# Optimization experiments

Hardware: AMD Instinct MI355X
Metric: run time of the kernel (lower is better)

Reference implementation:

```python
import jax, jax.numpy as jnp
import numpy as np

H = 128  # hidden_size


def lstm_layer(x, Wih, Whh, bih, bhh):
    """Unidirectional LSTM layer, batch_first input x: [B, T, I] -> [B, T, H].
    PyTorch gate order: i, f, g, o."""
    B = x.shape[0]
    # precompute input projections as one big GEMM: [B, T, 4H]
    xp = jnp.einsum('bti,gi->btg', x, Wih) + bih + bhh
    xp = jnp.transpose(xp, (1, 0, 2))  # [T, B, 4H]
    h0 = jnp.zeros((B, H), x.dtype)
    c0 = jnp.zeros((B, H), x.dtype)

    def step(carry, xp_t):
        h, c = carry
        gates = xp_t + h @ Whh.T  # [B, 4H]
        i, f, g, o = jnp.split(gates, 4, axis=-1)
        i = jax.nn.sigmoid(i)
        f = jax.nn.sigmoid(f)
        g = jnp.tanh(g)
        o = jax.nn.sigmoid(o)
        c = f * c + i * g
        h = o * jnp.tanh(c)
        return (h, c), h

    (_, _), ys = jax.lax.scan(step, (h0, c0), xp)
    return jnp.transpose(ys, (1, 0, 2))  # [B, T, H]


def setup_inputs() -> dict:
    key = jax.random.key(0)
    ks = jax.random.split(key, 13)
    s = 0.05
    inp = {
        'x': jax.random.normal(ks[0], (8, 1, 102400), jnp.float32),
        'Wih0': jax.random.normal(ks[1], (4 * H, 1), jnp.float32) * s,
        'Whh0': jax.random.normal(ks[2], (4 * H, H), jnp.float32) * s,
        'bih0': jnp.zeros((4 * H,), jnp.float32),
        'bhh0': jnp.zeros((4 * H,), jnp.float32).at[H:2 * H].set(1.0),
        'Wih1': jax.random.normal(ks[3], (4 * H, H), jnp.float32) * s,
        'Whh1': jax.random.normal(ks[4], (4 * H, H), jnp.float32) * s,
        'bih1': jnp.zeros((4 * H,), jnp.float32),
        'bhh1': jnp.zeros((4 * H,), jnp.float32).at[H:2 * H].set(1.0),
        'fcW1': jax.random.normal(ks[5], (H // 2, H), jnp.float32) * s,
        'fcb1': jnp.zeros((H // 2,), jnp.float32),
        'fcW2': jax.random.normal(ks[6], (11, H // 2), jnp.float32) * s,
        'fcb2': jnp.zeros((11,), jnp.float32),
    }
    return inp


def reference(x, Wih0, Whh0, bih0, bhh0, Wih1, Whh1, bih1, bhh1,
              fcW1, fcb1, fcW2, fcb2):
    # x: [B, 1, L] -> [B, L, 1]  (transpose(1, 2))
    x = jnp.transpose(x, (0, 2, 1))
    h1 = lstm_layer(x, Wih0, Whh0, bih0, bhh0)   # [B, T, H]
    h2 = lstm_layer(h1, Wih1, Whh1, bih1, bhh1)  # [B, T, H]
    pooled = jnp.mean(h2, axis=1)                # [B, H]; dropout is identity in eval
    hid = jax.nn.relu(pooled @ fcW1.T + fcb1)    # [B, H//2]
    logits = hid @ fcW2.T + fcb2                 # [B, 11]
    return logits
```

## Files before the change

kernel.cpp:

```cpp
#include <hip/hip_runtime.h>

#define HH 128
#define G4 512
#define TT 102400
#define BB 8

typedef _Float16 v2h __attribute__((ext_vector_type(2)));

#if __has_builtin(__builtin_amdgcn_fdot2)
#define FDOT2(a, b, c) __builtin_amdgcn_fdot2((a), (b), (c), false)
#else
static __device__ __forceinline__ float fdot2_fb(v2h a, v2h b, float c) {
    return fmaf((float)a[0], (float)b[0], fmaf((float)a[1], (float)b[1], c));
}
#define FDOT2(a, b, c) fdot2_fb((a), (b), (c))
#endif

template<int CTRL>
__device__ __forceinline__ float dpp_mov(float v) {
    return __int_as_float(
        __builtin_amdgcn_update_dpp(0, __float_as_int(v), CTRL, 0xF, 0xF, true));
}

__device__ __forceinline__ float tanh_f(float x) {
    return fmaf(2.0f, __builtin_amdgcn_rcpf(1.0f + __expf(-2.0f * x)), -1.0f);
}

static __device__ __forceinline__ void bar_lds() {
    __builtin_amdgcn_sched_barrier(0);
    asm volatile("s_waitcnt lgkmcnt(0)" ::: "memory");
    __builtin_amdgcn_s_barrier();
    __builtin_amdgcn_sched_barrier(0);
}

union HI { int i; v2h h; };

__device__ __forceinline__ float dotred(const v2h w[8][8],
                                        const _Float16* __restrict__ hsl,
                                        bool bp1, bool bp2, bool bp3) {
    const int4* hp4 = (const int4*)hsl;
    int4 ha = hp4[0], hb = hp4[1];
    int hp[8] = {ha.x, ha.y, ha.z, ha.w, hb.x, hb.y, hb.z, hb.w};
    float acc[8];
#pragma unroll
    for (int r = 0; r < 8; ++r) acc[r] = 0.f;
#pragma unroll
    for (int i = 0; i < 8; ++i) {
        HI u; u.i = hp[i];
#pragma unroll
        for (int r = 0; r < 8; ++r) acc[r] = FDOT2(w[r][i], u.h, acc[r]);
    }
    float b0[4];
#pragma unroll
    for (int m = 0; m < 4; ++m) {
        float send = bp1 ? acc[2 * m] : acc[2 * m + 1];
        float keep = bp1 ? acc[2 * m + 1] : acc[2 * m];
        b0[m] = keep + dpp_mov<0xB1>(send);
    }
    float d0[2];
#pragma unroll
    for (int i = 0; i < 2; ++i) {
        float send = bp2 ? b0[i] : b0[i + 2];
        float keep = bp2 ? b0[i + 2] : b0[i];
        d0[i] = keep + dpp_mov<0x4E>(send);
    }
    float send = bp3 ? d0[0] : d0[1];
    float keep = bp3 ? d0[1] : d0[0];
    return keep + dpp_mov<0x141>(send);
}

__device__ __forceinline__ void load_w8h(const float* __restrict__ W,
                                         int Q, int j, v2h w[8][8]) {
#pragma unroll
    for (int r = 0; r < 8; ++r) {
        int row = 2 * Q + (r & 1) + 128 * (r >> 1);
        const float4* rp = (const float4*)(W + (size_t)row * HH + 16 * j);
#pragma unroll
        for (int i = 0; i < 4; ++i) {
            float4 f = rp[i];
            w[r][2 * i]     = (v2h){(_Float16)f.x, (_Float16)f.y};
            w[r][2 * i + 1] = (v2h){(_Float16)f.z, (_Float16)f.w};
        }
    }
}

__global__ void __launch_bounds__(512, 2)
lstm_slot_kernel(
    const float* __restrict__ x,
    const float* __restrict__ Wih0, const float* __restrict__ Whh0,
    const float* __restrict__ bih0, const float* __restrict__ bhh0,
    const float* __restrict__ Wih1, const float* __restrict__ Whh1,
    const float* __restrict__ bih1, const float* __restrict__ bhh1,
    float* __restrict__ h1s, float* __restrict__ c1s,
    float* __restrict__ h2s, float* __restrict__ c2s,
    double* __restrict__ pooled,
    _Float16* __restrict__ h1ring,
    float* __restrict__ xpring,
    int c, int chunkT, int nchunks)
{
    __shared__ __align__(32) _Float16 hh[2 * HH];
    const int t = threadIdx.x;
    const int Q = t >> 3;
    const int j = t & 7;
    const bool bp1 = ((j ^ (j >> 2)) & 1) != 0;
    const bool bp2 = ((j ^ (j >> 1)) & 1) != 0;
    const bool bp3 = ((j >> 2) & 1) != 0;
    const int cellj = bp1 ? 1 : 0;
    const int gatej = (bp2 ? 2 : 0) + (bp3 ? 1 : 0);
    const int myc   = 2 * Q + cellj;
    const int myrow = myc + 128 * gatej;
    const bool owner = (gatej == 0);
    const bool isg = (gatej == 2);
    const float fe = isg ? -2.f : -1.f;
    const float fm = isg ?  2.f :  1.f;
    const float fa = isg ? -1.f :  0.f;

    if (blockIdx.x < 16) {
        const bool isA = (blockIdx.x < 8);
        const int cc = isA ? c : (c - 2);
        if (cc < 0 || cc >= nchunks) return;
        const int b = blockIdx.x & 7;

        v2h w[8][8];
        load_w8h(isA ? Whh0 : Whh1, Q, j, w);
        float bias_l = 0.f, wih_l = 0.f;
        if (isA) { bias_l = bih0[myrow] + bhh0[myrow]; wih_l = Wih0[myrow]; }

        float* hst = isA ? h1s : h2s;
        float* cst = isA ? c1s : c2s;
        float c_reg = cst[b * HH + myc];
        if (t < HH) hh[t] = (_Float16)hst[b * HH + t];

        _Float16* ringp = h1ring + ((size_t)((c & 1) * BB + b)) * (size_t)chunkT * HH;
        const float4* xb4 = (const float4*)(x + (size_t)b * TT + (size_t)cc * chunkT);
        const float* xps = xpring
            + ((size_t)((cc & 1) * BB + b)) * (size_t)chunkT * G4 + 4 * myc + gatej;

        const int nt4 = chunkT >> 2;
        float4 xq = {0, 0, 0, 0};
        float xpc[4] = {0, 0, 0, 0};
        if (isA) xq = xb4[0];
        else {
#pragma unroll
            for (int u = 0; u < 4; ++u) xpc[u] = xps[(size_t)u * G4];
        }
        double pacc = 0.0;
        float hfin = 0.f;
        bar_lds();

        for (int t4 = 0; t4 < nt4; ++t4) {
            float4 xqn = {0, 0, 0, 0};
            float xpn[4] = {0, 0, 0, 0};
            if (isA) {
                if (t4 + 1 < nt4) xqn = xb4[t4 + 1];
            } else if (t4 + 1 < nt4) {
#pragma unroll
                for (int u = 0; u < 4; ++u)
                    xpn[u] = xps[(size_t)(t4 * 4 + 4 + u) * G4];
            }
#pragma unroll
            for (int u = 0; u < 4; ++u) {
                const int buf = u & 1;
                float sfin = dotred(w, hh + buf * HH + 16 * j, bp1, bp2, bp3);
                float pre;
                if (isA) {
                    float xt = (u == 0) ? xq.x : (u == 1) ? xq.y
                             : (u == 2) ? xq.z : xq.w;
                    pre = fmaf(xt, wih_l, sfin + bias_l);
                } else {
                    pre = sfin + xpc[u];
                }
                float e  = __expf(pre * fe);
                float rr = __builtin_amdgcn_rcpf(1.0f + e);
                float act = fmaf(fm, rr, fa);
                float t1 = dpp_mov<0x141>(act);
                float t2 = dpp_mov<0x4E>(act);
                float t3 = dpp_mov<0x4E>(t1);
                c_reg = fmaf(t1, c_reg, act * t2);
                float th = tanh_f(c_reg);
                float hv = t3 * th;
                hfin = hv;
                if (owner) {
                    hh[(buf ^ 1) * HH + myc] = (_Float16)hv;
                    if (isA) ringp[(size_t)(t4 * 4 + u) * HH + myc] = (_Float16)hv;
                    else     pacc += (double)hv;
                }
                bar_lds();
            }
            xq = xqn;
            if (!isA) {
#pragma unroll
                for (int u = 0; u < 4; ++u) xpc[u] = xpn[u];
            }
        }
        if (owner) {
            cst[b * HH + myc] = c_reg;
            hst[b * HH + myc] = hfin;
            if (!isA) pooled[b * HH + myc] += pacc;
        }

    } else {
        const int bc = c - 1;
        if (bc < 0 || bc >= nchunks) return;
        const int ib = blockIdx.x - 16;
        const int bb = ib >> 3;
        const int sl = ib & 7;
        v2h w[8][8];
        load_w8h(Wih1, Q, j, w);
        const float bias_l = bih1[myrow] + bhh1[myrow];
        const _Float16* hrp = h1ring
            + ((size_t)((bc & 1) * BB + bb)) * (size_t)chunkT * HH;
        float* xpw = xpring + ((size_t)((bc & 1) * BB + bb)) * (size_t)chunkT * G4;
        if (t < HH) hh[t] = hrp[(size_t)sl * HH + t];
        bar_lds();
        int pb = 0;
        for (int tt = sl; tt < chunkT; tt += 8) {
            int ttn = tt + 8;
            bool pf = (t < HH) && (ttn < chunkT);
            _Float16 hn = (_Float16)0.f;
            if (pf) hn = hrp[(size_t)ttn * HH + t];
            float sfin = dotred(w, hh + pb * HH + 16 * j, bp1, bp2, bp3);
            if (pf) hh[(pb ^ 1) * HH + t] = hn;
            xpw[(size_t)tt * G4 + 4 * myc + gatej] = sfin + bias_l;
            bar_lds();
            pb ^= 1;
        }
    }
}

__global__ void head_kernel(const double* __restrict__ pooled,
                            const float* __restrict__ fcW1, const float* __restrict__ fcb1,
                            const float* __restrict__ fcW2, const float* __restrict__ fcb2,
                            float* __restrict__ out)
{
    __shared__ float p_s[HH];
    __shared__ float hid_s[64];
    const int b = blockIdx.x, t = threadIdx.x;
    if (t < HH) p_s[t] = (float)(pooled[b * HH + t] * (1.0 / (double)TT));
    __syncthreads();
    if (t < 64) {
        float acc = fcb1[t];
#pragma unroll 8
        for (int k = 0; k < HH; ++k) acc = fmaf(p_s[k], fcW1[t * HH + k], acc);
        hid_s[t] = fmaxf(acc, 0.f);
    }
    __syncthreads();
    if (t < 11) {
        float acc = fcb2[t];
#pragma unroll
        for (int k = 0; k < 64; ++k) acc = fmaf(hid_s[k], fcW2[t * 64 + k], acc);
        out[b * 11 + t] = acc;
    }
}

extern "C" void kernel_launch(void* const* d_in, const int* in_sizes, int n_in,
                              void* d_out, int out_size, void* d_ws, size_t ws_size,
                              hipStream_t stream)
{
    const float* x    = (const float*)d_in[0];
    const float* Wih0 = (const float*)d_in[1];
    const float* Whh0 = (const float*)d_in[2];
    const float* bih0 = (const float*)d_in[3];
    const float* bhh0 = (const float*)d_in[4];
    const float* Wih1 = (const float*)d_in[5];
    const float* Whh1 = (const float*)d_in[6];
    const float* bih1 = (const float*)d_in[7];
    const float* bhh1 = (const float*)d_in[8];
    const float* fcW1 = (const float*)d_in[9];
    const float* fcb1 = (const float*)d_in[10];
    const float* fcW2 = (const float*)d_in[11];
    const float* fcb2 = (const float*)d_in[12];
    float* out = (float*)d_out;

    char* wsp = (char*)d_ws;
    float*  h1s    = (float*) (wsp + 0);
    float*  c1s    = (float*) (wsp + 4096);
    float*  h2s    = (float*) (wsp + 8192);
    float*  c2s    = (float*) (wsp + 12288);
    double* pooled = (double*)(wsp + 16384);
    const size_t STATE_BYTES = 24576;

    static const int cands[] = {800, 400, 160, 80, 40, 8};
    int chunkT = 8;
    for (int i = 0; i < 6; ++i) {
        size_t need = STATE_BYTES + (size_t)36864 * (size_t)cands[i];
        if (need <= ws_size) { chunkT = cands[i]; break; }
    }
    const int nchunks = TT / chunkT;

    _Float16* h1ring = (_Float16*)(wsp + STATE_BYTES);
    float* xpring = (float*)(wsp + STATE_BYTES + (size_t)2 * BB * chunkT * HH * 2);

    hipMemsetAsync(d_ws, 0, STATE_BYTES, stream);

    const int nslots = nchunks + 2;
    for (int c = 0; c < nslots; ++c) {
        lstm_slot_kernel<<<80, 512, 0, stream>>>(
            x, Wih0, Whh0, bih0, bhh0, Wih1, Whh1, bih1, bhh1,
            h1s, c1s, h2s, c2s, pooled, h1ring, xpring,
            c, chunkT, nchunks);
    }
    head_kernel<<<BB, 128, 0, stream>>>(pooled, fcW1, fcb1, fcW2, fcb2, out);
}
```

Before: 57.92 ms.

## Compute recurrent LSTM matvec with MFMA 16x16x32 instead of fdot2 lane reductions

The recurrent blocks now compute h·Whh with MFMA 16x16x32 f16 instructions. Each wave holds fp16 weight fragments for 16 cells across all four gates. One active lane per cell extracts its four gate sums and runs the full cell update, which replaces the fdot2-plus-DPP cross-lane reduction and the DPP gate exchange. The custom LDS barrier is replaced by __syncthreads and the xprojection prefetch is reorganised per step pair. This trades the reduction latency for MFMA latency on a serial chain, with only a quarter of lanes doing activations.

```diff
diff --git a/kernel.cpp b/kernel.cpp
--- a/kernel.cpp
+++ b/kernel.cpp
@@ -6,6 +6,10 @@
 #define BB 8
 
 typedef _Float16 v2h __attribute__((ext_vector_type(2)));
+typedef _Float16 v8h __attribute__((ext_vector_type(8)));
+typedef float    f4v __attribute__((ext_vector_type(4)));
+
+#define MFMA16(A, B, C) __builtin_amdgcn_mfma_f32_16x16x32_f16((A), (B), (C), 0, 0, 0)
 
 #if __has_builtin(__builtin_amdgcn_fdot2)
 #define FDOT2(a, b, c) __builtin_amdgcn_fdot2((a), (b), (c), false)
@@ -25,12 +29,8 @@
 __device__ __forceinline__ float tanh_f(float x) {
     return fmaf(2.0f, __builtin_amdgcn_rcpf(1.0f + __expf(-2.0f * x)), -1.0f);
 }
-
-static __device__ __forceinline__ void bar_lds() {
-    __builtin_amdgcn_sched_barrier(0);
-    asm volatile("s_waitcnt lgkmcnt(0)" ::: "memory");
-    __builtin_amdgcn_s_barrier();
-    __builtin_amdgcn_sched_barrier(0);
+__device__ __forceinline__ float sigm_f(float x) {
+    return __builtin_amdgcn_rcpf(1.0f + __expf(-x));
 }
 
 union HI { int i; v2h h; };
@@ -100,20 +100,6 @@
 {
     __shared__ __align__(32) _Float16 hh[2 * HH];
     const int t = threadIdx.x;
-    const int Q = t >> 3;
-    const int j = t & 7;
-    const bool bp1 = ((j ^ (j >> 2)) & 1) != 0;
-    const bool bp2 = ((j ^ (j >> 1)) & 1) != 0;
-    const bool bp3 = ((j >> 2) & 1) != 0;
-    const int cellj = bp1 ? 1 : 0;
-    const int gatej = (bp2 ? 2 : 0) + (bp3 ? 1 : 0);
-    const int myc   = 2 * Q + cellj;
-    const int myrow = myc + 128 * gatej;
-    const bool owner = (gatej == 0);
-    const bool isg = (gatej == 2);
-    const float fe = isg ? -2.f : -1.f;
-    const float fm = isg ?  2.f :  1.f;
-    const float fa = isg ? -1.f :  0.f;
 
     if (blockIdx.x < 16) {
         const bool isA = (blockIdx.x < 8);
@@ -121,87 +107,155 @@
         if (cc < 0 || cc >= nchunks) return;
         const int b = blockIdx.x & 7;
 
-        v2h w[8][8];
-        load_w8h(isA ? Whh0 : Whh1, Q, j, w);
-        float bias_l = 0.f, wih_l = 0.f;
-        if (isA) { bias_l = bih0[myrow] + bhh0[myrow]; wih_l = Wih0[myrow]; }
+        const int l   = t & 63;
+        const int wv  = t >> 6;
+        const int lhi = l >> 4;
+        const int lq  = l & 3;
+        const int koff = 8 * lhi;
+        const bool act_lane = ((l & 12) == 0);
+        const int cellw = 16 * wv + 4 * lhi + lq;
+        const bool s0_ = (l & 1) != 0, s1_ = (l & 2) != 0;
+
+        const float* Wc = isA ? Whh0 : Whh1;
+        v8h af[4][4];
+#pragma unroll
+        for (int g = 0; g < 4; ++g) {
+            const float* wr = Wc + (size_t)(16 * wv + 128 * g + (l & 15)) * HH;
+#pragma unroll
+            for (int kt = 0; kt < 4; ++kt) {
+                const f4v* p = (const f4v*)(wr + 32 * kt + koff);
+                f4v fa = p[0], fb = p[1];
+                v8h v;
+                v[0] = (_Float16)fa[0]; v[1] = (_Float16)fa[1];
+                v[2] = (_Float16)fa[2]; v[3] = (_Float16)fa[3];
+                v[4] = (_Float16)fb[0]; v[5] = (_Float16)fb[1];
+                v[6] = (_Float16)fb[2]; v[7] = (_Float16)fb[3];
+                af[g][kt] = v;
+            }
+        }
+        f4v cin[4] = {{0,0,0,0},{0,0,0,0},{0,0,0,0},{0,0,0,0}};
+        float wih_[4] = {0.f, 0.f, 0.f, 0.f};
+        if (isA) {
+#pragma unroll
+            for (int g = 0; g < 4; ++g) {
+#pragma unroll
+                for (int r = 0; r < 4; ++r) {
+                    int row = 16 * wv + 128 * g + 4 * lhi + r;
+                    cin[g][r] = bih0[row] + bhh0[row];
+                }
+                wih_[g] = Wih0[cellw + 128 * g];
+            }
+        }
 
         float* hst = isA ? h1s : h2s;
         float* cst = isA ? c1s : c2s;
-        float c_reg = cst[b * HH + myc];
+        float c_reg = cst[b * HH + cellw];
         if (t < HH) hh[t] = (_Float16)hst[b * HH + t];
 
-        _Float16* ringp = h1ring + ((size_t)((c & 1) * BB + b)) * (size_t)chunkT * HH;
-        const float4* xb4 = (const float4*)(x + (size_t)b * TT + (size_t)cc * chunkT);
-        const float* xps = xpring
-            + ((size_t)((cc & 1) * BB + b)) * (size_t)chunkT * G4 + 4 * myc + gatej;
-
-        const int nt4 = chunkT >> 2;
-        float4 xq = {0, 0, 0, 0};
-        float xpc[4] = {0, 0, 0, 0};
-        if (isA) xq = xb4[0];
-        else {
-#pragma unroll
-            for (int u = 0; u < 4; ++u) xpc[u] = xps[(size_t)u * G4];
-        }
+        _Float16* rp = h1ring + ((size_t)((c & 1) * BB + b)) * (size_t)chunkT * HH;
+        const float* xrow = x + (size_t)b * TT + (size_t)cc * chunkT;
+        const float* xpp = xpring
+            + ((size_t)((cc & 1) * BB + b)) * (size_t)chunkT * G4 + 4 * cellw;
+
+        float xt0 = 0.f, xt1 = 0.f;
+        f4v xp0 = {0,0,0,0}, xp1 = {0,0,0,0};
+        if (isA) { xt0 = xrow[0]; xt1 = xrow[1]; }
+        else if (act_lane) {
+            xp0 = *(const f4v*)(xpp);
+            xp1 = *(const f4v*)(xpp + G4);
+        }
+        const float* xrp = xrow + 2;
+        const float* xpn = xpp + 2 * (size_t)G4;
+
         double pacc = 0.0;
         float hfin = 0.f;
-        bar_lds();
-
-        for (int t4 = 0; t4 < nt4; ++t4) {
-            float4 xqn = {0, 0, 0, 0};
-            float xpn[4] = {0, 0, 0, 0};
+        __syncthreads();
+
+#define CHAIN_STEP(PAR, XT, XP) do {                                          \
+        const _Float16* hb_ = hh + (PAR) * HH + koff;                         \
+        v8h b0_ = *(const v8h*)(hb_);                                         \
+        v8h b1_ = *(const v8h*)(hb_ + 32);                                    \
+        v8h b2_ = *(const v8h*)(hb_ + 64);                                    \
+        v8h b3_ = *(const v8h*)(hb_ + 96);                                    \
+        f4v a0_ = MFMA16(af[0][0], b0_, cin[0]);                              \
+        f4v a1_ = MFMA16(af[1][0], b0_, cin[1]);                              \
+        f4v a2_ = MFMA16(af[2][0], b0_, cin[2]);                              \
+        f4v a3_ = MFMA16(af[3][0], b0_, cin[3]);                              \
+        a0_ = MFMA16(af[0][1], b1_, a0_); a1_ = MFMA16(af[1][1], b1_, a1_);   \
+        a2_ = MFMA16(af[2][1], b1_, a2_); a3_ = MFMA16(af[3][1], b1_, a3_);   \
+        a0_ = MFMA16(af[0][2], b2_, a0_); a1_ = MFMA16(af[1][2], b2_, a1_);   \
+        a2_ = MFMA16(af[2][2], b2_, a2_); a3_ = MFMA16(af[3][2], b2_, a3_);   \
+        a0_ = MFMA16(af[0][3], b3_, a0_); a1_ = MFMA16(af[1][3], b3_, a1_);   \
+        a2_ = MFMA16(af[2][3], b3_, a2_); a3_ = MFMA16(af[3][3], b3_, a3_);   \
+        float q01_, q23_, si_, sf_, sg2_, so_;                                \
+        q01_ = s0_ ? a0_[1] : a0_[0]; q23_ = s0_ ? a0_[3] : a0_[2];           \
+        si_  = s1_ ? q23_ : q01_;                                             \
+        q01_ = s0_ ? a1_[1] : a1_[0]; q23_ = s0_ ? a1_[3] : a1_[2];           \
+        sf_  = s1_ ? q23_ : q01_;                                             \
+        q01_ = s0_ ? a2_[1] : a2_[0]; q23_ = s0_ ? a2_[3] : a2_[2];           \
+        sg2_ = s1_ ? q23_ : q01_;                                             \
+        q01_ = s0_ ? a3_[1] : a3_[0]; q23_ = s0_ ? a3_[3] : a3_[2];           \
+        so_  = s1_ ? q23_ : q01_;                                             \
+        if (act_lane) {                                                       \
+            float pi_, pf_, pg_, po_;                                         \
+            if (isA) {                                                        \
+                pi_ = fmaf(XT, wih_[0], si_);                                 \
+                pf_ = fmaf(XT, wih_[1], sf_);                                 \
+                pg_ = fmaf(XT, wih_[2], sg2_);                                \
+                po_ = fmaf(XT, wih_[3], so_);                                 \
+            } else {                                                          \
+                pi_ = si_ + XP[0]; pf_ = sf_ + XP[1];                         \
+                pg_ = sg2_ + XP[2]; po_ = so_ + XP[3];                        \
+            }                                                                 \
+            float gi_ = sigm_f(pi_), gf_ = sigm_f(pf_);                       \
+            float gg_ = tanh_f(pg_), go_ = sigm_f(po_);                       \
+            c_reg = fmaf(gf_, c_reg, gi_ * gg_);                              \
+            float hv_ = go_ * tanh_f(c_reg);                                  \
+            hfin = hv_;                                                       \
+            hh[(((PAR) ^ 1)) * HH + cellw] = (_Float16)hv_;                   \
+            if (isA) rp[cellw] = (_Float16)hv_;                               \
+            else     pacc += (double)hv_;                                     \
+        }                                                                     \
+        rp += HH;                                                             \
+        __syncthreads();                                                      \
+    } while (0)
+
+        for (int s = 0; s < chunkT; s += 2) {
+            float xt2 = 0.f, xt3 = 0.f;
+            f4v xp2 = {0,0,0,0}, xp3 = {0,0,0,0};
+            const bool p2 = (s + 2 < chunkT);
             if (isA) {
-                if (t4 + 1 < nt4) xqn = xb4[t4 + 1];
-            } else if (t4 + 1 < nt4) {
-#pragma unroll
-                for (int u = 0; u < 4; ++u)
-                    xpn[u] = xps[(size_t)(t4 * 4 + 4 + u) * G4];
+                if (p2) { xt2 = xrp[0]; xt3 = xrp[1]; }
+            } else if (act_lane && p2) {
+                xp2 = *(const f4v*)(xpn);
+                xp3 = *(const f4v*)(xpn + G4);
             }
-#pragma unroll
-            for (int u = 0; u < 4; ++u) {
-                const int buf = u & 1;
-                float sfin = dotred(w, hh + buf * HH + 16 * j, bp1, bp2, bp3);
-                float pre;
-                if (isA) {
-                    float xt = (u == 0) ? xq.x : (u == 1) ? xq.y
-                             : (u == 2) ? xq.z : xq.w;
-                    pre = fmaf(xt, wih_l, sfin + bias_l);
-                } else {
-                    pre = sfin + xpc[u];
-                }
-                float e  = __expf(pre * fe);
-                float rr = __builtin_amdgcn_rcpf(1.0f + e);
-                float act = fmaf(fm, rr, fa);
-                float t1 = dpp_mov<0x141>(act);
-                float t2 = dpp_mov<0x4E>(act);
-                float t3 = dpp_mov<0x4E>(t1);
-                c_reg = fmaf(t1, c_reg, act * t2);
-                float th = tanh_f(c_reg);
-                float hv = t3 * th;
-                hfin = hv;
-                if (owner) {
-                    hh[(buf ^ 1) * HH + myc] = (_Float16)hv;
-                    if (isA) ringp[(size_t)(t4 * 4 + u) * HH + myc] = (_Float16)hv;
-                    else     pacc += (double)hv;
-                }
-                bar_lds();
-            }
-            xq = xqn;
-            if (!isA) {
-#pragma unroll
-                for (int u = 0; u < 4; ++u) xpc[u] = xpn[u];
-            }
-        }
-        if (owner) {
-            cst[b * HH + myc] = c_reg;
-            hst[b * HH + myc] = hfin;
-            if (!isA) pooled[b * HH + myc] += pacc;
+            CHAIN_STEP(0, xt0, xp0);
+            CHAIN_STEP(1, xt1, xp1);
+            xt0 = xt2; xt1 = xt3; xp0 = xp2; xp1 = xp3;
+            xrp += 2; xpn += 2 * (size_t)G4;
+        }
+#undef CHAIN_STEP
+
+        if (act_lane) {
+            cst[b * HH + cellw] = c_reg;
+            hst[b * HH + cellw] = hfin;
+            if (!isA) pooled[b * HH + cellw] += pacc;
         }
 
     } else {
         const int bc = c - 1;
         if (bc < 0 || bc >= nchunks) return;
+        const int Q = t >> 3;
+        const int j = t & 7;
+        const bool bp1 = ((j ^ (j >> 2)) & 1) != 0;
+        const bool bp2 = ((j ^ (j >> 1)) & 1) != 0;
+        const bool bp3 = ((j >> 2) & 1) != 0;
+        const int cellj = bp1 ? 1 : 0;
+        const int gatej = (bp2 ? 2 : 0) + (bp3 ? 1 : 0);
+        const int myc   = 2 * Q + cellj;
+        const int myrow = myc + 128 * gatej;
+
         const int ib = blockIdx.x - 16;
         const int bb = ib >> 3;
         const int sl = ib & 7;
@@ -212,7 +266,7 @@
             + ((size_t)((bc & 1) * BB + bb)) * (size_t)chunkT * HH;
         float* xpw = xpring + ((size_t)((bc & 1) * BB + bb)) * (size_t)chunkT * G4;
         if (t < HH) hh[t] = hrp[(size_t)sl * HH + t];
-        bar_lds();
+        __syncthreads();
         int pb = 0;
         for (int tt = sl; tt < chunkT; tt += 8) {
             int ttn = tt + 8;
@@ -222,7 +276,7 @@
             float sfin = dotred(w, hh + pb * HH + 16 * j, bp1, bp2, bp3);
             if (pf) hh[(pb ^ 1) * HH + t] = hn;
             xpw[(size_t)tt * G4 + 4 * myc + gatej] = sfin + bias_l;
-            bar_lds();
+            __syncthreads();
             pb ^= 1;
         }
     }
```

New measurement: 59.50 ms. 2.7% more time.

## Batch all sequences per recurrent block and compute recurrence with MFMA

Applied to the files above, without the earlier changes.

The recurrent layer blocks now handle all 8 batch rows in a single 256-thread workgroup, using 16x16x32 f16 MFMA instructions with Whh held in registers as A-fragments, in place of one 512-thread block per batch row using fdot2 and DPP reductions. Each lane evaluates the gate nonlinearities for 4 cells directly, and x is staged into LDS for the chunk. The layer-1 input-projection blocks are split into two halves over cells, giving 130 blocks of 256 threads. This trades per-step cross-lane reduction work and many blocks for a denser matrix-core step with one barrier. The risk is a longer per-step serial MFMA dependency chain on a single CU per layer.

```diff
diff --git a/kernel.cpp b/kernel.cpp
--- a/kernel.cpp
+++ b/kernel.cpp
@@ -4,8 +4,14 @@
 #define G4 512
 #define TT 102400
 #define BB 8
+#define XS 801
+#define HS2 144
 
 typedef _Float16 v2h __attribute__((ext_vector_type(2)));
+typedef _Float16 v8h __attribute__((ext_vector_type(8)));
+typedef float    f4v __attribute__((ext_vector_type(4)));
+
+#define MFMA16(A, B, C) __builtin_amdgcn_mfma_f32_16x16x32_f16((A), (B), (C), 0, 0, 0)
 
 #if __has_builtin(__builtin_amdgcn_fdot2)
 #define FDOT2(a, b, c) __builtin_amdgcn_fdot2((a), (b), (c), false)
@@ -25,12 +31,8 @@
 __device__ __forceinline__ float tanh_f(float x) {
     return fmaf(2.0f, __builtin_amdgcn_rcpf(1.0f + __expf(-2.0f * x)), -1.0f);
 }
-
-static __device__ __forceinline__ void bar_lds() {
-    __builtin_amdgcn_sched_barrier(0);
-    asm volatile("s_waitcnt lgkmcnt(0)" ::: "memory");
-    __builtin_amdgcn_s_barrier();
-    __builtin_amdgcn_sched_barrier(0);
+__device__ __forceinline__ float sigm_f(float x) {
+    return __builtin_amdgcn_rcpf(1.0f + __expf(-x));
 }
 
 union HI { int i; v2h h; };
@@ -70,10 +72,10 @@
 }
 
 __device__ __forceinline__ void load_w8h(const float* __restrict__ W,
-                                         int Q, int j, v2h w[8][8]) {
+                                         int Q, int j, int ch, v2h w[8][8]) {
 #pragma unroll
     for (int r = 0; r < 8; ++r) {
-        int row = 2 * Q + (r & 1) + 128 * (r >> 1);
+        int row = 64 * ch + 2 * Q + (r & 1) + 128 * (r >> 1);
         const float4* rp = (const float4*)(W + (size_t)row * HH + 16 * j);
 #pragma unroll
         for (int i = 0; i < 4; ++i) {
@@ -84,7 +86,7 @@
     }
 }
 
-__global__ void __launch_bounds__(512, 2)
+__global__ void __launch_bounds__(256, 1)
 lstm_slot_kernel(
     const float* __restrict__ x,
     const float* __restrict__ Wih0, const float* __restrict__ Whh0,
@@ -98,131 +100,258 @@
     float* __restrict__ xpring,
     int c, int chunkT, int nchunks)
 {
-    __shared__ __align__(32) _Float16 hh[2 * HH];
+    __shared__ __align__(16) _Float16 hh2[2][BB * HS2];
+    __shared__ __align__(16) float x_lds[BB * XS];
     const int t = threadIdx.x;
-    const int Q = t >> 3;
-    const int j = t & 7;
-    const bool bp1 = ((j ^ (j >> 2)) & 1) != 0;
-    const bool bp2 = ((j ^ (j >> 1)) & 1) != 0;
-    const bool bp3 = ((j >> 2) & 1) != 0;
-    const int cellj = bp1 ? 1 : 0;
-    const int gatej = (bp2 ? 2 : 0) + (bp3 ? 1 : 0);
-    const int myc   = 2 * Q + cellj;
-    const int myrow = myc + 128 * gatej;
-    const bool owner = (gatej == 0);
-    const bool isg = (gatej == 2);
-    const float fe = isg ? -2.f : -1.f;
-    const float fm = isg ?  2.f :  1.f;
-    const float fa = isg ? -1.f :  0.f;
-
-    if (blockIdx.x < 16) {
-        const bool isA = (blockIdx.x < 8);
+
+    if (blockIdx.x < 2) {
+        const bool isA = (blockIdx.x == 0);
         const int cc = isA ? c : (c - 2);
         if (cc < 0 || cc >= nchunks) return;
-        const int b = blockIdx.x & 7;
-
-        v2h w[8][8];
-        load_w8h(isA ? Whh0 : Whh1, Q, j, w);
-        float bias_l = 0.f, wih_l = 0.f;
-        if (isA) { bias_l = bih0[myrow] + bhh0[myrow]; wih_l = Wih0[myrow]; }
+
+        const int l   = t & 63;
+        const int w   = t >> 6;
+        const int lr  = l & 15;
+        const int lhi = l >> 4;
+        const int bb  = lr & 7;
+        const int hs  = lr >> 3;
+        const int ccb = 32 * w + 16 * hs + 4 * lhi;
+
+        const float* Wc = isA ? Whh0 : Whh1;
+        v8h af[4][2][4];
+#pragma unroll
+        for (int g = 0; g < 4; ++g)
+#pragma unroll
+            for (int h2 = 0; h2 < 2; ++h2)
+#pragma unroll
+                for (int kt = 0; kt < 4; ++kt) {
+                    const float* wr = Wc + (size_t)(32 * w + 16 * h2 + lr + 128 * g) * HH
+                                    + 32 * kt + 8 * lhi;
+                    f4v fa = *(const f4v*)wr, fb = *(const f4v*)(wr + 4);
+                    v8h v;
+                    v[0] = (_Float16)fa[0]; v[1] = (_Float16)fa[1];
+                    v[2] = (_Float16)fa[2]; v[3] = (_Float16)fa[3];
+                    v[4] = (_Float16)fb[0]; v[5] = (_Float16)fb[1];
+                    v[6] = (_Float16)fb[2]; v[7] = (_Float16)fb[3];
+                    af[g][h2][kt] = v;
+                }
+
+        f4v cin[4][2];
+#pragma unroll
+        for (int g = 0; g < 4; ++g)
+#pragma unroll
+            for (int h2 = 0; h2 < 2; ++h2) cin[g][h2] = (f4v){0.f, 0.f, 0.f, 0.f};
+        float wih[4][4];
+#pragma unroll
+        for (int r = 0; r < 4; ++r)
+#pragma unroll
+            for (int g = 0; g < 4; ++g) wih[r][g] = 0.f;
+        if (isA) {
+#pragma unroll
+            for (int g = 0; g < 4; ++g)
+#pragma unroll
+                for (int h2 = 0; h2 < 2; ++h2)
+#pragma unroll
+                    for (int r = 0; r < 4; ++r) {
+                        int row = 32 * w + 16 * h2 + 4 * lhi + r + 128 * g;
+                        cin[g][h2][r] = bih0[row] + bhh0[row];
+                    }
+#pragma unroll
+            for (int r = 0; r < 4; ++r)
+#pragma unroll
+                for (int g = 0; g < 4; ++g) wih[r][g] = Wih0[ccb + r + 128 * g];
+        }
 
         float* hst = isA ? h1s : h2s;
         float* cst = isA ? c1s : c2s;
-        float c_reg = cst[b * HH + myc];
-        if (t < HH) hh[t] = (_Float16)hst[b * HH + t];
-
-        _Float16* ringp = h1ring + ((size_t)((c & 1) * BB + b)) * (size_t)chunkT * HH;
-        const float4* xb4 = (const float4*)(x + (size_t)b * TT + (size_t)cc * chunkT);
+        float cr0 = cst[bb * HH + ccb + 0];
+        float cr1 = cst[bb * HH + ccb + 1];
+        float cr2 = cst[bb * HH + ccb + 2];
+        float cr3 = cst[bb * HH + ccb + 3];
+        float hl0 = 0.f, hl1 = 0.f, hl2 = 0.f, hl3 = 0.f;
+        float pac0 = 0.f, pac1 = 0.f, pac2 = 0.f, pac3 = 0.f;
+
+        for (int i = t; i < BB * HH; i += 256)
+            hh2[0][(i >> 7) * HS2 + (i & 127)] = (_Float16)hst[i];
+        if (isA) {
+            for (int b_ = 0; b_ < 8; ++b_)
+                for (int tp = t; tp < chunkT; tp += 256)
+                    x_lds[b_ * XS + tp] = x[(size_t)b_ * TT + (size_t)cc * chunkT + tp];
+        }
+
+        _Float16* rp = h1ring + ((size_t)((c & 1) * BB + bb)) * (size_t)chunkT * HH + ccb;
         const float* xps = xpring
-            + ((size_t)((cc & 1) * BB + b)) * (size_t)chunkT * G4 + 4 * myc + gatej;
-
-        const int nt4 = chunkT >> 2;
-        float4 xq = {0, 0, 0, 0};
-        float xpc[4] = {0, 0, 0, 0};
-        if (isA) xq = xb4[0];
-        else {
-#pragma unroll
-            for (int u = 0; u < 4; ++u) xpc[u] = xps[(size_t)u * G4];
-        }
-        double pacc = 0.0;
-        float hfin = 0.f;
-        bar_lds();
-
-        for (int t4 = 0; t4 < nt4; ++t4) {
-            float4 xqn = {0, 0, 0, 0};
-            float xpn[4] = {0, 0, 0, 0};
-            if (isA) {
-                if (t4 + 1 < nt4) xqn = xb4[t4 + 1];
-            } else if (t4 + 1 < nt4) {
-#pragma unroll
-                for (int u = 0; u < 4; ++u)
-                    xpn[u] = xps[(size_t)(t4 * 4 + 4 + u) * G4];
-            }
-#pragma unroll
-            for (int u = 0; u < 4; ++u) {
-                const int buf = u & 1;
-                float sfin = dotred(w, hh + buf * HH + 16 * j, bp1, bp2, bp3);
-                float pre;
-                if (isA) {
-                    float xt = (u == 0) ? xq.x : (u == 1) ? xq.y
-                             : (u == 2) ? xq.z : xq.w;
-                    pre = fmaf(xt, wih_l, sfin + bias_l);
-                } else {
-                    pre = sfin + xpc[u];
-                }
-                float e  = __expf(pre * fe);
-                float rr = __builtin_amdgcn_rcpf(1.0f + e);
-                float act = fmaf(fm, rr, fa);
-                float t1 = dpp_mov<0x141>(act);
-                float t2 = dpp_mov<0x4E>(act);
-                float t3 = dpp_mov<0x4E>(t1);
-                c_reg = fmaf(t1, c_reg, act * t2);
-                float th = tanh_f(c_reg);
-                float hv = t3 * th;
-                hfin = hv;
-                if (owner) {
-                    hh[(buf ^ 1) * HH + myc] = (_Float16)hv;
-                    if (isA) ringp[(size_t)(t4 * 4 + u) * HH + myc] = (_Float16)hv;
-                    else     pacc += (double)hv;
-                }
-                bar_lds();
-            }
-            xq = xqn;
-            if (!isA) {
-#pragma unroll
-                for (int u = 0; u < 4; ++u) xpc[u] = xpn[u];
-            }
-        }
-        if (owner) {
-            cst[b * HH + myc] = c_reg;
-            hst[b * HH + myc] = hfin;
-            if (!isA) pooled[b * HH + myc] += pacc;
+            + ((size_t)((cc & 1) * BB + bb)) * (size_t)chunkT * G4 + 4 * ccb;
+
+        f4v xc0 = {0,0,0,0}, xc1 = {0,0,0,0}, xc2 = {0,0,0,0}, xc3 = {0,0,0,0};
+        f4v xn0 = {0,0,0,0}, xn1 = {0,0,0,0}, xn2 = {0,0,0,0}, xn3 = {0,0,0,0};
+        if (!isA) {
+            xc0 = *(const f4v*)(xps);     xc1 = *(const f4v*)(xps + 4);
+            xc2 = *(const f4v*)(xps + 8); xc3 = *(const f4v*)(xps + 12);
+        }
+        __syncthreads();
+
+#define CSTEP(PB, S, SN, XC0,XC1,XC2,XC3, XN0,XN1,XN2,XN3) do {               \
+        if (!isA && (SN) < chunkT) {                                          \
+            const float* q_ = xps + (size_t)(SN) * G4;                        \
+            XN0 = *(const f4v*)q_;        XN1 = *(const f4v*)(q_ + 4);        \
+            XN2 = *(const f4v*)(q_ + 8);  XN3 = *(const f4v*)(q_ + 12);       \
+        }                                                                     \
+        const _Float16* hb_ = &hh2[PB][bb * HS2 + 8 * lhi];                   \
+        v8h B0_ = *(const v8h*)(hb_);                                         \
+        v8h B1_ = *(const v8h*)(hb_ + 32);                                    \
+        v8h B2_ = *(const v8h*)(hb_ + 64);                                    \
+        v8h B3_ = *(const v8h*)(hb_ + 96);                                    \
+        f4v a00_ = cin[0][0], a01_ = cin[0][1], a10_ = cin[1][0],             \
+            a11_ = cin[1][1], a20_ = cin[2][0], a21_ = cin[2][1],             \
+            a30_ = cin[3][0], a31_ = cin[3][1];                               \
+        a00_ = MFMA16(af[0][0][0], B0_, a00_);                                \
+        a00_ = MFMA16(af[0][0][1], B1_, a00_);                                \
+        a00_ = MFMA16(af[0][0][2], B2_, a00_);                                \
+        a00_ = MFMA16(af[0][0][3], B3_, a00_);                                \
+        a10_ = MFMA16(af[1][0][0], B0_, a10_);                                \
+        a10_ = MFMA16(af[1][0][1], B1_, a10_);                                \
+        a10_ = MFMA16(af[1][0][2], B2_, a10_);                                \
+        a10_ = MFMA16(af[1][0][3], B3_, a10_);                                \
+        a20_ = MFMA16(af[2][0][0], B0_, a20_);                                \
+        a20_ = MFMA16(af[2][0][1], B1_, a20_);                                \
+        a20_ = MFMA16(af[2][0][2], B2_, a20_);                                \
+        a20_ = MFMA16(af[2][0][3], B3_, a20_);                                \
+        a30_ = MFMA16(af[3][0][0], B0_, a30_);                                \
+        a30_ = MFMA16(af[3][0][1], B1_, a30_);                                \
+        a30_ = MFMA16(af[3][0][2], B2_, a30_);                                \
+        a30_ = MFMA16(af[3][0][3], B3_, a30_);                                \
+        a01_ = MFMA16(af[0][1][0], B0_, a01_);                                \
+        a01_ = MFMA16(af[0][1][1], B1_, a01_);                                \
+        a01_ = MFMA16(af[0][1][2], B2_, a01_);                                \
+        a01_ = MFMA16(af[0][1][3], B3_, a01_);                                \
+        a11_ = MFMA16(af[1][1][0], B0_, a11_);                                \
+        a11_ = MFMA16(af[1][1][1], B1_, a11_);                                \
+        a11_ = MFMA16(af[1][1][2], B2_, a11_);                                \
+        a11_ = MFMA16(af[1][1][3], B3_, a11_);                                \
+        a21_ = MFMA16(af[2][1][0], B0_, a21_);                                \
+        a21_ = MFMA16(af[2][1][1], B1_, a21_);                                \
+        a21_ = MFMA16(af[2][1][2], B2_, a21_);                                \
+        a21_ = MFMA16(af[2][1][3], B3_, a21_);                                \
+        a31_ = MFMA16(af[3][1][0], B0_, a31_);                                \
+        a31_ = MFMA16(af[3][1][1], B1_, a31_);                                \
+        a31_ = MFMA16(af[3][1][2], B2_, a31_);                                \
+        a31_ = MFMA16(af[3][1][3], B3_, a31_);                                \
+        f4v vi_ = hs ? a01_ : a00_;  f4v vf_ = hs ? a11_ : a10_;              \
+        f4v vg_ = hs ? a21_ : a20_;  f4v vo_ = hs ? a31_ : a30_;              \
+        float xt_ = x_lds[bb * XS + (S)];                                     \
+        float h0_, h1_, h2v_, h3_;                                            \
+        {                                                                     \
+            float pi_, pf_, pg_, po_;                                         \
+            if (isA) { pi_ = fmaf(xt_, wih[0][0], vi_[0]);                    \
+                       pf_ = fmaf(xt_, wih[0][1], vf_[0]);                    \
+                       pg_ = fmaf(xt_, wih[0][2], vg_[0]);                    \
+                       po_ = fmaf(xt_, wih[0][3], vo_[0]); }                  \
+            else { pi_ = vi_[0] + XC0[0]; pf_ = vf_[0] + XC0[1];              \
+                   pg_ = vg_[0] + XC0[2]; po_ = vo_[0] + XC0[3]; }            \
+            float gi_ = sigm_f(pi_), gf_ = sigm_f(pf_);                       \
+            float gg_ = tanh_f(pg_), go_ = sigm_f(po_);                       \
+            cr0 = fmaf(gf_, cr0, gi_ * gg_);  h0_ = go_ * tanh_f(cr0);        \
+        }                                                                     \
+        {                                                                     \
+            float pi_, pf_, pg_, po_;                                         \
+            if (isA) { pi_ = fmaf(xt_, wih[1][0], vi_[1]);                    \
+                       pf_ = fmaf(xt_, wih[1][1], vf_[1]);                    \
+                       pg_ = fmaf(xt_, wih[1][2], vg_[1]);                    \
+                       po_ = fmaf(xt_, wih[1][3], vo_[1]); }                  \
+            else { pi_ = vi_[1] + XC1[0]; pf_ = vf_[1] + XC1[1];              \
+                   pg_ = vg_[1] + XC1[2]; po_ = vo_[1] + XC1[3]; }            \
+            float gi_ = sigm_f(pi_), gf_ = sigm_f(pf_);                       \
+            float gg_ = tanh_f(pg_), go_ = sigm_f(po_);                       \
+            cr1 = fmaf(gf_, cr1, gi_ * gg_);  h1_ = go_ * tanh_f(cr1);        \
+        }                                                                     \
+        {                                                                     \
+            float pi_, pf_, pg_, po_;                                         \
+            if (isA) { pi_ = fmaf(xt_, wih[2][0], vi_[2]);                    \
+                       pf_ = fmaf(xt_, wih[2][1], vf_[2]);                    \
+                       pg_ = fmaf(xt_, wih[2][2], vg_[2]);                    \
+                       po_ = fmaf(xt_, wih[2][3], vo_[2]); }                  \
+            else { pi_ = vi_[2] + XC2[0]; pf_ = vf_[2] + XC2[1];              \
+                   pg_ = vg_[2] + XC2[2]; po_ = vo_[2] + XC2[3]; }            \
+            float gi_ = sigm_f(pi_), gf_ = sigm_f(pf_);                       \
+            float gg_ = tanh_f(pg_), go_ = sigm_f(po_);                       \
+            cr2 = fmaf(gf_, cr2, gi_ * gg_);  h2v_ = go_ * tanh_f(cr2);       \
+        }                                                                     \
+        {                                                                     \
+            float pi_, pf_, pg_, po_;                                         \
+            if (isA) { pi_ = fmaf(xt_, wih[3][0], vi_[3]);                    \
+                       pf_ = fmaf(xt_, wih[3][1], vf_[3]);                    \
+                       pg_ = fmaf(xt_, wih[3][2], vg_[3]);                    \
+                       po_ = fmaf(xt_, wih[3][3], vo_[3]); }                  \
+            else { pi_ = vi_[3] + XC3[0]; pf_ = vf_[3] + XC3[1];              \
+                   pg_ = vg_[3] + XC3[2]; po_ = vo_[3] + XC3[3]; }            \
+            float gi_ = sigm_f(pi_), gf_ = sigm_f(pf_);                       \
+            float gg_ = tanh_f(pg_), go_ = sigm_f(po_);                       \
+            cr3 = fmaf(gf_, cr3, gi_ * gg_);  h3_ = go_ * tanh_f(cr3);        \
+        }                                                                     \
+        union { v2h hp[2]; unsigned long long u; } pk_;                       \
+        pk_.hp[0] = (v2h){(_Float16)h0_, (_Float16)h1_};                      \
+        pk_.hp[1] = (v2h){(_Float16)h2v_, (_Float16)h3_};                     \
+        *(unsigned long long*)(&hh2[(PB) ^ 1][bb * HS2 + ccb]) = pk_.u;       \
+        if (isA) *(unsigned long long*)(rp + (size_t)(S) * HH) = pk_.u;       \
+        else { pac0 += h0_; pac1 += h1_; pac2 += h2v_; pac3 += h3_; }         \
+        hl0 = h0_; hl1 = h1_; hl2 = h2v_; hl3 = h3_;                          \
+        __syncthreads();                                                      \
+    } while (0)
+
+        for (int s = 0; s < chunkT; s += 2) {
+            CSTEP(0, s,     s + 1, xc0, xc1, xc2, xc3, xn0, xn1, xn2, xn3);
+            CSTEP(1, s + 1, s + 2, xn0, xn1, xn2, xn3, xc0, xc1, xc2, xc3);
+        }
+#undef CSTEP
+
+        cst[bb * HH + ccb + 0] = cr0; cst[bb * HH + ccb + 1] = cr1;
+        cst[bb * HH + ccb + 2] = cr2; cst[bb * HH + ccb + 3] = cr3;
+        hst[bb * HH + ccb + 0] = hl0; hst[bb * HH + ccb + 1] = hl1;
+        hst[bb * HH + ccb + 2] = hl2; hst[bb * HH + ccb + 3] = hl3;
+        if (!isA) {
+            pooled[bb * HH + ccb + 0] += (double)pac0;
+            pooled[bb * HH + ccb + 1] += (double)pac1;
+            pooled[bb * HH + ccb + 2] += (double)pac2;
+            pooled[bb * HH + ccb + 3] += (double)pac3;
         }
 
     } else {
         const int bc = c - 1;
         if (bc < 0 || bc >= nchunks) return;
-        const int ib = blockIdx.x - 16;
-        const int bb = ib >> 3;
-        const int sl = ib & 7;
-        v2h w[8][8];
-        load_w8h(Wih1, Q, j, w);
+        const int ib = blockIdx.x - 2;
+        const int bb2 = ib >> 4;
+        const int sl = (ib >> 1) & 7;
+        const int ch = ib & 1;
+        const int Q = t >> 3;
+        const int j = t & 7;
+        const bool bp1 = ((j ^ (j >> 2)) & 1) != 0;
+        const bool bp2 = ((j ^ (j >> 1)) & 1) != 0;
+        const bool bp3 = ((j >> 2) & 1) != 0;
+        const int cellj = bp1 ? 1 : 0;
+        const int gatej = (bp2 ? 2 : 0) + (bp3 ? 1 : 0);
+        const int myc   = 64 * ch + 2 * Q + cellj;
+        const int myrow = myc + 128 * gatej;
+
+        v2h wB[8][8];
+        load_w8h(Wih1, Q, j, ch, wB);
         const float bias_l = bih1[myrow] + bhh1[myrow];
         const _Float16* hrp = h1ring
-            + ((size_t)((bc & 1) * BB + bb)) * (size_t)chunkT * HH;
-        float* xpw = xpring + ((size_t)((bc & 1) * BB + bb)) * (size_t)chunkT * G4;
-        if (t < HH) hh[t] = hrp[(size_t)sl * HH + t];
-        bar_lds();
+            + ((size_t)((bc & 1) * BB + bb2)) * (size_t)chunkT * HH;
+        float* xpw = xpring + ((size_t)((bc & 1) * BB + bb2)) * (size_t)chunkT * G4;
+        _Float16* hhB = &hh2[0][0];
+        if (t < HH) hhB[t] = hrp[(size_t)sl * HH + t];
+        __syncthreads();
         int pb = 0;
         for (int tt = sl; tt < chunkT; tt += 8) {
             int ttn = tt + 8;
             bool pf = (t < HH) && (ttn < chunkT);
             _Float16 hn = (_Float16)0.f;
             if (pf) hn = hrp[(size_t)ttn * HH + t];
-            float sfin = dotred(w, hh + pb * HH + 16 * j, bp1, bp2, bp3);
-            if (pf) hh[(pb ^ 1) * HH + t] = hn;
+            float sfin = dotred(wB, hhB + pb * HH + 16 * j, bp1, bp2, bp3);
+            if (pf) hhB[(pb ^ 1) * HH + t] = hn;
             xpw[(size_t)tt * G4 + 4 * myc + gatej] = sfin + bias_l;
-            bar_lds();
+            __syncthreads();
             pb ^= 1;
         }
     }
@@ -295,7 +424,7 @@
 
     const int nslots = nchunks + 2;
     for (int c = 0; c < nslots; ++c) {
-        lstm_slot_kernel<<<80, 512, 0, stream>>>(
+        lstm_slot_kernel<<<130, 256, 0, stream>>>(
             x, Wih0, Whh0, bih0, bhh0, Wih1, Whh1, bih1, bhh1,
             h1s, c1s, h2s, c2s, pooled, h1ring, xpring,
             c, chunkT, nchunks);
```

Result: slower. 100.9 ms (+74.2%).
